# Kernel optimization log

Hardware: AMD Instinct MI355X
Metric: run time of the kernel (lower is better)

The kernel has to match this reference:

```python
import jax, jax.numpy as jnp
import numpy as np

EPS_COS = 1e-8   # nxn_cos_sim eps
SMOOTH = 1e-4    # DiceLoss smooth
EPS_DICE = 1e-7  # smp soft_dice_score clamp_min eps

BS, C, H, W = 8, 512, 128, 128
K = 512  # codebook / num classes


def setup_inputs() -> dict:
    key = jax.random.key(0)
    k1, k2, k3 = jax.random.split(key, 3)
    output = jax.random.normal(k1, (BS, C, H, W), dtype=jnp.float32)
    embeddings = jax.random.normal(k2, (K, C), dtype=jnp.float32)
    # ground-truth one-hot annotation (bs, K, h, w)
    gt_labels = jax.random.randint(k3, (BS, H, W), 0, K)
    ann_one_hot = jax.nn.one_hot(gt_labels, K, dtype=jnp.float32).transpose(0, 3, 1, 2)
    return {"output": output, "ann_one_hot": ann_one_hot, "embeddings": embeddings}


def reference(output, ann_one_hot, embeddings):
    bs, c, h, w = output.shape
    k = embeddings.shape[0]
    x = output.transpose(0, 2, 3, 1).reshape(-1, c)           # [N, C]
    # nxn cosine similarity [N, K]
    numerator = x @ embeddings.T
    a_l2 = jnp.sum(x * x, axis=1)                              # [N]
    b_l2 = jnp.sum(embeddings * embeddings, axis=1)            # [K]
    denominator = jnp.maximum(jnp.sqrt(a_l2[:, None] * b_l2[None, :]), EPS_COS)
    labels = jnp.argmax(numerator / denominator, axis=-1).reshape(bs, h, w)
    # ann_to_one_hot -> (bs, K, h, w)
    pred_one_hot = jax.nn.one_hot(labels, k, dtype=output.dtype).transpose(0, 3, 1, 2)
    # smp DiceLoss(mode='multilabel', smooth=1e-4, from_logits=False)
    yp = pred_one_hot.reshape(bs, k, -1)
    yt = ann_one_hot.reshape(bs, k, -1).astype(yp.dtype)
    dims = (0, 2)
    intersection = jnp.sum(yp * yt, axis=dims)                 # [K]
    cardinality = jnp.sum(yp + yt, axis=dims)                  # [K]
    score = (2.0 * intersection + SMOOTH) / jnp.maximum(cardinality + SMOOTH, EPS_DICE)
    loss = 1.0 - score
    present = (jnp.sum(yt, axis=dims) > 0).astype(loss.dtype)  # only classes present in GT
    return jnp.mean(loss * present)
```

## Files before the change

### kernel.cpp

```cpp
#include <hip/hip_runtime.h>
#include <hip/hip_bf16.h>

#define BSZ 8
#define CDIM 512
#define KDIM 512
#define HWSZ 16384
#define NPIX (BSZ*HWSZ)

using bf16x8 = __attribute__((ext_vector_type(8))) short;
using f32x4  = __attribute__((ext_vector_type(4))) float;
typedef unsigned long long u64;

__device__ __forceinline__ unsigned pack2bf16(float lo, float hi) {
  return (__builtin_bit_cast(unsigned, lo) >> 16) |
         (__builtin_bit_cast(unsigned, hi) & 0xFFFF0000u);
}

__device__ __forceinline__ void gload_lds16(const unsigned short* g, unsigned short* l) {
  __builtin_amdgcn_global_load_lds(
      (const __attribute__((address_space(1))) unsigned int*)g,
      (__attribute__((address_space(3))) unsigned int*)l, 16, 0, 0);
}

__global__ __launch_bounds__(64) void prep_emb_kernel(const float* __restrict__ E,
                                                      unsigned short* __restrict__ Eb,
                                                      unsigned short* __restrict__ EbT,
                                                      u64* __restrict__ keys,
                                                      float* __restrict__ counters,
                                                      int do_keys) {
  int k = blockIdx.x;
  int lane = threadIdx.x;
  if (do_keys) {
    u64* kp = keys + (size_t)k * 256;
    #pragma unroll
    for (int j = 0; j < 4; ++j) kp[lane + 64 * j] = 0ull;
  }
  if (k == 0) {
    uint4 z = {0u, 0u, 0u, 0u};
    #pragma unroll
    for (int j = 0; j < 6; ++j) ((uint4*)counters)[lane + 64 * j] = z;
  }
  const float4* row = (const float4*)(E + (size_t)k * CDIM);
  float4 v0 = row[lane * 2], v1 = row[lane * 2 + 1];
  float ss = v0.x*v0.x + v0.y*v0.y + v0.z*v0.z + v0.w*v0.w
           + v1.x*v1.x + v1.y*v1.y + v1.z*v1.z + v1.w*v1.w;
  #pragma unroll
  for (int d = 1; d < 64; d <<= 1) ss += __shfl_xor(ss, d, 64);
  float rinv = rsqrtf(fmaxf(ss, 1e-24f));
  float f[8] = {v0.x, v0.y, v0.z, v0.w, v1.x, v1.y, v1.z, v1.w};
  unsigned o[8];
  #pragma unroll
  for (int e = 0; e < 8; ++e) {
    float x = f[e] * rinv;
    unsigned u = __builtin_bit_cast(unsigned, x);
    o[e] = (u + 0x7FFFu + ((u >> 16) & 1u)) >> 16;
  }
  uint4 pack;
  pack.x = o[0] | (o[1] << 16);
  pack.y = o[2] | (o[3] << 16);
  pack.z = o[4] | (o[5] << 16);
  pack.w = o[6] | (o[7] << 16);
  ((uint4*)(Eb + (size_t)k * CDIM))[lane] = pack;
  int clsb = k >> 7, rowi = k & 127, cs = lane >> 2, q4 = lane & 3;
  *(uint4*)(EbT + (size_t)clsb * 65536 + cs * 4096 + rowi * 32 + q4 * 8) = pack;
}

__global__ __launch_bounds__(256) void gt_count_kernel(const float* __restrict__ ANN,
                                                       float* __restrict__ gt_count) {
  int slice = blockIdx.x;
  int k = slice & (KDIM - 1);
  const float4* p = (const float4*)(ANN + (size_t)slice * HWSZ);
  float s = 0.f;
  #pragma unroll
  for (int i = 0; i < 16; ++i) {
    float4 v = p[threadIdx.x + i * 256];
    s += v.x + v.y + v.z + v.w;
  }
  #pragma unroll
  for (int d = 1; d < 64; d <<= 1) s += __shfl_xor(s, d, 64);
  __shared__ float sw[4];
  if ((threadIdx.x & 63) == 0) sw[threadIdx.x >> 6] = s;
  __syncthreads();
  if (threadIdx.x == 0) {
    atomicAdd(&gt_count[k], sw[0] + sw[1] + sw[2] + sw[3]);
  }
}

__global__ __launch_bounds__(256) void transpose_v3_kernel(
    const float* __restrict__ X, unsigned short* __restrict__ XtT) {
  __shared__ unsigned int lds[16 * 1024];
  int t = threadIdx.x, w = t >> 6, l = t & 63;
  int bid = blockIdx.x;
  int pt = bid >> 4, ks = bid & 15;
  int px0 = pt << 10;
  int b = px0 >> 14, hw = px0 & (HWSZ - 1);
  const float* xb = X + ((size_t)b * CDIM + ks * 32 + 8 * w) * HWSZ + hw + 4 * l;

  float4 xv[8][4];
  #pragma unroll
  for (int r = 0; r < 8; ++r)
    #pragma unroll
    for (int s = 0; s < 4; ++s)
      xv[r][s] = *(const float4*)(xb + (size_t)r * HWSZ + s * 256);

  #pragma unroll
  for (int rp = 0; rp < 4; ++rp) {
    int cp = 4 * w + rp;
    int swz = (cp & 7) << 2;
    #pragma unroll
    for (int s = 0; s < 4; ++s) {
      unsigned pk[4];
      #pragma unroll
      for (int j = 0; j < 4; ++j)
        pk[j] = pack2bf16(((const float*)&xv[2 * rp][s])[j],
                          ((const float*)&xv[2 * rp + 1][s])[j]);
      *(uint4*)&lds[cp * 1024 + ((s * 256 + 4 * l) ^ swz)] = *(const uint4*)pk;
    }
  }
  __syncthreads();

  #pragma unroll
  for (int rr = 0; rr < 16; ++rr) {
    int ch = rr * 256 + t;
    int q4 = ch & 3, pxl = ch >> 2;
    unsigned o[4];
    #pragma unroll
    for (int j = 0; j < 4; ++j) {
      int cp = 4 * q4 + j;
      o[j] = lds[cp * 1024 + (pxl ^ ((cp & 7) << 2))];
    }
    int pxg = px0 + pxl;
    *(uint4*)(XtT + ((size_t)(pxg >> 7) * 16 + ks) * 4096 + (size_t)(pxg & 127) * 32 + q4 * 8)
        = *(const uint4*)o;
  }
}

__global__ __launch_bounds__(256, 4) void gemm_argmax_kernel(
    const unsigned short* __restrict__ XtT, const unsigned short* __restrict__ EbT,
    u64* __restrict__ keys) {
  __shared__ unsigned short As[2][128 * 32];
  __shared__ unsigned short Bs[2][128 * 32];
  int t = threadIdx.x;
  int lane = t & 63;
  int wv = t >> 6;
  int p15 = lane & 15, q = lane >> 4;
  int wr = wv >> 1, wc = wv & 1;
  int bid = (blockIdx.x & 7) * 512 + (blockIdx.x >> 3);
  int pxb  = bid >> 2;
  int clsb = bid & 3;
  int px0  = pxb * 128;
  int cls0 = clsb * 128;

  const unsigned short* Abase = XtT + (size_t)pxb * 65536;
  const unsigned short* Bbase = EbT + (size_t)clsb * 65536;
  int ubase = (t & ~63) * 8;
  #define STAGE(buf, i)                                                       \
    {                                                                         \
      _Pragma("unroll")                                                       \
      for (int j = 0; j < 2; ++j) {                                           \
        int ch = t + 256 * j;                                                 \
        gload_lds16(Abase + (size_t)(i) * 4096 + ch * 8, &As[buf][ubase + j * 2048]); \
        gload_lds16(Bbase + (size_t)(i) * 4096 + ch * 8, &Bs[buf][ubase + j * 2048]); \
      }                                                                       \
    }

  f32x4 acc[4][4];
  #pragma unroll
  for (int m = 0; m < 4; ++m)
    #pragma unroll
    for (int n = 0; n < 4; ++n)
      acc[m][n] = (f32x4){0.f, 0.f, 0.f, 0.f};

  STAGE(0, 0);
  for (int i = 0; i < 16; ++i) {
    int cur = i & 1;
    if (i < 15) STAGE(cur ^ 1, i + 1);
    __syncthreads();
    bf16x8 a[4], bfr[4];
    #pragma unroll
    for (int m = 0; m < 4; ++m)
      a[m] = *(bf16x8*)&As[cur][(wr * 64 + m * 16 + p15) * 32 + q * 8];
    #pragma unroll
    for (int n = 0; n < 4; ++n)
      bfr[n] = *(bf16x8*)&Bs[cur][(wc * 64 + n * 16 + p15) * 32 + q * 8];
    #pragma unroll
    for (int n = 0; n < 4; ++n)
      #pragma unroll
      for (int m = 0; m < 4; ++m)
        acc[m][n] = __builtin_amdgcn_mfma_f32_16x16x32_bf16(a[m], bfr[n], acc[m][n], 0, 0, 0);
    __syncthreads();
  }
  #undef STAGE

  #pragma unroll
  for (int m = 0; m < 4; ++m) {
    #pragma unroll
    for (int r = 0; r < 4; ++r) {
      float best = acc[m][0][r];
      int bn = 0;
      #pragma unroll
      for (int n = 1; n < 4; ++n) {
        float v = acc[m][n][r];
        if (v > best) { best = v; bn = n; }
      }
      int bk = cls0 + wc * 64 + bn * 16 + p15;
      #pragma unroll
      for (int d = 1; d < 16; d <<= 1) {
        float ov = __shfl_xor(best, d, 64);
        int   ok = __shfl_xor(bk, d, 64);
        if (ov > best || (ov == best && ok < bk)) { best = ov; bk = ok; }
      }
      if (p15 == 0) {
        int px = px0 + wr * 64 + m * 16 + q * 4 + r;
        unsigned u = __builtin_bit_cast(unsigned, best);
        unsigned ou = u ^ ((unsigned)((int)u >> 31) | 0x80000000u);
        u64 key = ((u64)ou << 32) | (unsigned)(511 - bk);
        atomicMax(&keys[px], key);
      }
    }
  }
}

__global__ __launch_bounds__(256) void count_kernel(
    const u64* __restrict__ keys, const float* __restrict__ ANN,
    int* __restrict__ pred_count, int* __restrict__ inter) {
  int px = blockIdx.x * 256 + threadIdx.x;
  u64 key = keys[px];
  int cls = 511 - (int)(unsigned)(key & 0xFFFFFFFFull);
  atomicAdd(&pred_count[cls], 1);
  int b = px >> 14, hw = px & (HWSZ - 1);
  float g = ANN[((size_t)b * KDIM + cls) * HWSZ + hw];
  if (g > 0.5f) atomicAdd(&inter[cls], 1);
}

__global__ __launch_bounds__(512) void final_kernel(
    const int* __restrict__ pred_count, const int* __restrict__ inter,
    const float* __restrict__ gt_count, float* __restrict__ out) {
  int k = threadIdx.x;
  float G = gt_count[k];
  float P = (float)pred_count[k];
  float I = (float)inter[k];
  float card  = P + G;
  float score = (2.f * I + 1e-4f) / fmaxf(card + 1e-4f, 1e-7f);
  float v = (G > 0.f) ? (1.f - score) : 0.f;
  #pragma unroll
  for (int d = 1; d < 64; d <<= 1) v += __shfl_xor(v, d, 64);
  __shared__ float sw[8];
  if ((k & 63) == 0) sw[k >> 6] = v;
  __syncthreads();
  if (k == 0) {
    float s = 0.f;
    #pragma unroll
    for (int i = 0; i < 8; ++i) s += sw[i];
    out[0] = s / (float)KDIM;
  }
}

__global__ __launch_bounds__(256, 1) void gemm_fb(
    const float* __restrict__ X, const float* __restrict__ ANN,
    const unsigned short* __restrict__ Eb,
    int* __restrict__ pred_count, int* __restrict__ inter) {
  int tid = threadIdx.x;
  int wv = tid >> 6;
  int lane = tid & 63;
  int p15 = lane & 15, q = lane >> 4;
  int pix0 = blockIdx.x * 64;
  int b = pix0 >> 14;
  int hw = pix0 & (HWSZ - 1);
  const float*          Xb = X  + (size_t)b * CDIM * HWSZ + hw + p15;
  const unsigned short* Ew = Eb + (size_t)(wv * 128) * CDIM;
  f32x4 acc[4][8];
  #pragma unroll
  for (int m = 0; m < 4; ++m)
    #pragma unroll
    for (int n = 0; n < 8; ++n)
      acc[m][n] = (f32x4){0.f, 0.f, 0.f, 0.f};
  for (int cs = 0; cs < 16; ++cs) {
    int c0 = cs * 32 + q * 8;
    bf16x8 a[4];
    #pragma unroll
    for (int m = 0; m < 4; ++m)
      #pragma unroll
      for (int e = 0; e < 8; ++e) {
        float x = Xb[(size_t)(c0 + e) * HWSZ + m * 16];
        a[m][e] = (short)(__builtin_bit_cast(unsigned, x) >> 16);
      }
    bf16x8 bfrag[8];
    #pragma unroll
    for (int n = 0; n < 8; ++n)
      bfrag[n] = *(const bf16x8*)(Ew + (size_t)(n * 16 + p15) * CDIM + cs * 32 + q * 8);
    #pragma unroll
    for (int n = 0; n < 8; ++n)
      #pragma unroll
      for (int m = 0; m < 4; ++m)
        acc[m][n] = __builtin_amdgcn_mfma_f32_16x16x32_bf16(a[m], bfrag[n], acc[m][n], 0, 0, 0);
  }
  __shared__ float s_v[4][64];
  __shared__ int   s_k[4][64];
  #pragma unroll
  for (int m = 0; m < 4; ++m)
    #pragma unroll
    for (int r = 0; r < 4; ++r) {
      float best = acc[m][0][r];
      int bn = 0;
      #pragma unroll
      for (int n = 1; n < 8; ++n) {
        float v = acc[m][n][r];
        if (v > best) { best = v; bn = n; }
      }
      int bk = wv * 128 + bn * 16 + p15;
      #pragma unroll
      for (int d = 1; d < 16; d <<= 1) {
        float ov = __shfl_xor(best, d, 64);
        int   ok = __shfl_xor(bk, d, 64);
        if (ov > best || (ov == best && ok < bk)) { best = ov; bk = ok; }
      }
      if (p15 == 0) {
        int p = m * 16 + q * 4 + r;
        s_v[wv][p] = best;
        s_k[wv][p] = bk;
      }
    }
  __syncthreads();
  if (tid < 64) {
    int p = tid;
    float best = s_v[0][p]; int bk = s_k[0][p];
    #pragma unroll
    for (int w = 1; w < 4; ++w) {
      float v = s_v[w][p]; int kk = s_k[w][p];
      if (v > best || (v == best && kk < bk)) { best = v; bk = kk; }
    }
    atomicAdd(&pred_count[bk], 1);
    float g = ANN[((size_t)b * KDIM + bk) * HWSZ + hw + p];
    if (g > 0.5f) atomicAdd(&inter[bk], 1);
  }
}

extern "C" void kernel_launch(void* const* d_in, const int* in_sizes, int n_in,
                              void* d_out, int out_size, void* d_ws, size_t ws_size,
                              hipStream_t stream) {
  const float* X   = (const float*)d_in[0];
  const float* ANN = (const float*)d_in[1];
  const float* E   = (const float*)d_in[2];

  char* base = (char*)d_ws;
  unsigned short* Eb  = (unsigned short*)base;
  unsigned short* EbT = (unsigned short*)(base + 524288);
  float* gt_count     = (float*)(base + 1048576);
  int*   pred_count   = (int*)  (base + 1048576 + 2048);
  int*   inter        = (int*)  (base + 1048576 + 4096);
  u64*   keys         = (u64*)  (base + 1048576 + 8192);
  unsigned short* XtT = (unsigned short*)(base + 4194304);

  size_t need = 4194304 + (size_t)NPIX * CDIM * 2;
  int big = (ws_size >= need) ? 1 : 0;

  prep_emb_kernel<<<KDIM, 64, 0, stream>>>(E, Eb, EbT, keys, gt_count, big);
  if (big) {
    gt_count_kernel<<<BSZ * KDIM, 256, 0, stream>>>(ANN, gt_count);
    transpose_v3_kernel<<<2048, 256, 0, stream>>>(X, XtT);
    gemm_argmax_kernel<<<4096, 256, 0, stream>>>(XtT, EbT, keys);
    count_kernel<<<NPIX / 256, 256, 0, stream>>>(keys, ANN, pred_count, inter);
  } else {
    gt_count_kernel<<<BSZ * KDIM, 256, 0, stream>>>(ANN, gt_count);
    gemm_fb<<<NPIX / 64, 256, 0, stream>>>(X, ANN, Eb, pred_count, inter);
  }
  final_kernel<<<1, 512, 0, stream>>>(pred_count, inter, gt_count, (float*)d_out);
}
```

Before: 286.6 us.

## Fuse GEMM-argmax, counting and GT-count into one kernel with full-K class tiles

```diff
diff --git a/kernel.cpp b/kernel.cpp
--- a/kernel.cpp
+++ b/kernel.cpp
@@ -25,16 +25,9 @@
 __global__ __launch_bounds__(64) void prep_emb_kernel(const float* __restrict__ E,
                                                       unsigned short* __restrict__ Eb,
                                                       unsigned short* __restrict__ EbT,
-                                                      u64* __restrict__ keys,
-                                                      float* __restrict__ counters,
-                                                      int do_keys) {
+                                                      float* __restrict__ counters) {
   int k = blockIdx.x;
   int lane = threadIdx.x;
-  if (do_keys) {
-    u64* kp = keys + (size_t)k * 256;
-    #pragma unroll
-    for (int j = 0; j < 4; ++j) kp[lane + 64 * j] = 0ull;
-  }
   if (k == 0) {
     uint4 z = {0u, 0u, 0u, 0u};
     #pragma unroll
@@ -61,8 +54,8 @@
   pack.z = o[4] | (o[5] << 16);
   pack.w = o[6] | (o[7] << 16);
   ((uint4*)(Eb + (size_t)k * CDIM))[lane] = pack;
-  int clsb = k >> 7, rowi = k & 127, cs = lane >> 2, q4 = lane & 3;
-  *(uint4*)(EbT + (size_t)clsb * 65536 + cs * 4096 + rowi * 32 + q4 * 8) = pack;
+  int ks = lane >> 2, q4 = lane & 3;
+  *(uint4*)(EbT + ((size_t)ks * 512 + k) * 32 + q4 * 8) = pack;
 }
 
 __global__ __launch_bounds__(256) void gt_count_kernel(const float* __restrict__ ANN,
@@ -81,9 +74,7 @@
   __shared__ float sw[4];
   if ((threadIdx.x & 63) == 0) sw[threadIdx.x >> 6] = s;
   __syncthreads();
-  if (threadIdx.x == 0) {
-    atomicAdd(&gt_count[k], sw[0] + sw[1] + sw[2] + sw[3]);
-  }
+  if (threadIdx.x == 0) atomicAdd(&gt_count[k], sw[0] + sw[1] + sw[2] + sw[3]);
 }
 
 __global__ __launch_bounds__(256) void transpose_v3_kernel(
@@ -130,38 +121,58 @@
       o[j] = lds[cp * 1024 + (pxl ^ ((cp & 7) << 2))];
     }
     int pxg = px0 + pxl;
-    *(uint4*)(XtT + ((size_t)(pxg >> 7) * 16 + ks) * 4096 + (size_t)(pxg & 127) * 32 + q4 * 8)
+    *(uint4*)(XtT + ((size_t)(pxg >> 6) * 16 + ks) * 2048 + (size_t)(pxg & 63) * 32 + q4 * 8)
         = *(const uint4*)o;
   }
 }
 
-__global__ __launch_bounds__(256, 4) void gemm_argmax_kernel(
+__global__ __launch_bounds__(512, 4) void mega_kernel(
     const unsigned short* __restrict__ XtT, const unsigned short* __restrict__ EbT,
-    u64* __restrict__ keys) {
-  __shared__ unsigned short As[2][128 * 32];
-  __shared__ unsigned short Bs[2][128 * 32];
+    const float* __restrict__ ANN, float* __restrict__ gt_count,
+    int* __restrict__ pred_count, int* __restrict__ inter) {
+  __shared__ unsigned short As[2][64 * 32];
+  __shared__ unsigned short Bs[2][512 * 32];
+  __shared__ float s_v[8][64];
+  __shared__ int   s_k[8][64];
+  __shared__ float sgt[8];
   int t = threadIdx.x;
-  int lane = t & 63;
-  int wv = t >> 6;
+  int bid = blockIdx.x;
+
+  if (bid & 1) {
+    int g = bid >> 1;
+    int which = t >> 8, tt = t & 255, w = t >> 6, lane = t & 63;
+    const float* Ap = ANN + (size_t)(2 * g + which) * HWSZ + tt * 4;
+    float s = 0.f;
+    #pragma unroll
+    for (int i = 0; i < 16; ++i) {
+      float4 v = *(const float4*)(Ap + (size_t)i * 1024);
+      s += (v.x + v.y) + (v.z + v.w);
+    }
+    #pragma unroll
+    for (int d = 1; d < 64; d <<= 1) s += __shfl_xor(s, d, 64);
+    if (lane == 0) sgt[w] = s;
+    __syncthreads();
+    if (t == 0)   atomicAdd(&gt_count[(2 * g)     & (KDIM - 1)], sgt[0] + sgt[1] + sgt[2] + sgt[3]);
+    if (t == 256) atomicAdd(&gt_count[(2 * g + 1) & (KDIM - 1)], sgt[4] + sgt[5] + sgt[6] + sgt[7]);
+    return;
+  }
+
+  int pxblk = bid >> 1;
+  int px0 = pxblk * 64;
+  int b = px0 >> 14, hw = px0 & (HWSZ - 1);
+  int lane = t & 63, wv = t >> 6;
   int p15 = lane & 15, q = lane >> 4;
-  int wr = wv >> 1, wc = wv & 1;
-  int bid = (blockIdx.x & 7) * 512 + (blockIdx.x >> 3);
-  int pxb  = bid >> 2;
-  int clsb = bid & 3;
-  int px0  = pxb * 128;
-  int cls0 = clsb * 128;
-
-  const unsigned short* Abase = XtT + (size_t)pxb * 65536;
-  const unsigned short* Bbase = EbT + (size_t)clsb * 65536;
-  int ubase = (t & ~63) * 8;
-  #define STAGE(buf, i)                                                       \
-    {                                                                         \
-      _Pragma("unroll")                                                       \
-      for (int j = 0; j < 2; ++j) {                                           \
-        int ch = t + 256 * j;                                                 \
-        gload_lds16(Abase + (size_t)(i) * 4096 + ch * 8, &As[buf][ubase + j * 2048]); \
-        gload_lds16(Bbase + (size_t)(i) * 4096 + ch * 8, &Bs[buf][ubase + j * 2048]); \
-      }                                                                       \
+
+  const unsigned short* Abase = XtT + (size_t)pxblk * 32768;
+  #define STAGE(buf, i)                                                               \
+    {                                                                                 \
+      _Pragma("unroll")                                                               \
+      for (int j = 0; j < 4; ++j)                                                     \
+        gload_lds16(EbT + (size_t)(i) * 16384 + ((size_t)t + 512 * j) * 8,            \
+                    &Bs[buf][(t & ~63) * 8 + j * 4096]);                              \
+      if (t < 256)                                                                    \
+        gload_lds16(Abase + (size_t)(i) * 2048 + (size_t)t * 8,                       \
+                    &As[buf][(t & ~63) * 8]);                                         \
     }
 
   f32x4 acc[4][4];
@@ -179,10 +190,10 @@
     bf16x8 a[4], bfr[4];
     #pragma unroll
     for (int m = 0; m < 4; ++m)
-      a[m] = *(bf16x8*)&As[cur][(wr * 64 + m * 16 + p15) * 32 + q * 8];
+      a[m] = *(bf16x8*)&As[cur][(m * 16 + p15) * 32 + q * 8];
     #pragma unroll
     for (int n = 0; n < 4; ++n)
-      bfr[n] = *(bf16x8*)&Bs[cur][(wc * 64 + n * 16 + p15) * 32 + q * 8];
+      bfr[n] = *(bf16x8*)&Bs[cur][(wv * 64 + n * 16 + p15) * 32 + q * 8];
     #pragma unroll
     for (int n = 0; n < 4; ++n)
       #pragma unroll
@@ -203,7 +214,7 @@
         float v = acc[m][n][r];
         if (v > best) { best = v; bn = n; }
       }
-      int bk = cls0 + wc * 64 + bn * 16 + p15;
+      int bk = wv * 64 + bn * 16 + p15;
       #pragma unroll
       for (int d = 1; d < 16; d <<= 1) {
         float ov = __shfl_xor(best, d, 64);
@@ -211,26 +222,25 @@
         if (ov > best || (ov == best && ok < bk)) { best = ov; bk = ok; }
       }
       if (p15 == 0) {
-        int px = px0 + wr * 64 + m * 16 + q * 4 + r;
-        unsigned u = __builtin_bit_cast(unsigned, best);
-        unsigned ou = u ^ ((unsigned)((int)u >> 31) | 0x80000000u);
-        u64 key = ((u64)ou << 32) | (unsigned)(511 - bk);
-        atomicMax(&keys[px], key);
-      }
-    }
-  }
-}
-
-__global__ __launch_bounds__(256) void count_kernel(
-    const u64* __restrict__ keys, const float* __restrict__ ANN,
-    int* __restrict__ pred_count, int* __restrict__ inter) {
-  int px = blockIdx.x * 256 + threadIdx.x;
-  u64 key = keys[px];
-  int cls = 511 - (int)(unsigned)(key & 0xFFFFFFFFull);
-  atomicAdd(&pred_count[cls], 1);
-  int b = px >> 14, hw = px & (HWSZ - 1);
-  float g = ANN[((size_t)b * KDIM + cls) * HWSZ + hw];
-  if (g > 0.5f) atomicAdd(&inter[cls], 1);
+        int p = m * 16 + q * 4 + r;
+        s_v[wv][p] = best;
+        s_k[wv][p] = bk;
+      }
+    }
+  }
+  __syncthreads();
+  if (t < 64) {
+    int p = t;
+    float best = s_v[0][p]; int bk = s_k[0][p];
+    #pragma unroll
+    for (int w = 1; w < 8; ++w) {
+      float v = s_v[w][p]; int kk = s_k[w][p];
+      if (v > best || (v == best && kk < bk)) { best = v; bk = kk; }
+    }
+    atomicAdd(&pred_count[bk], 1);
+    float g2 = ANN[((size_t)b * KDIM + bk) * HWSZ + hw + p];
+    if (g2 > 0.5f) atomicAdd(&inter[bk], 1);
+  }
 }
 
 __global__ __launch_bounds__(512) void final_kernel(
@@ -349,18 +359,15 @@
   float* gt_count     = (float*)(base + 1048576);
   int*   pred_count   = (int*)  (base + 1048576 + 2048);
   int*   inter        = (int*)  (base + 1048576 + 4096);
-  u64*   keys         = (u64*)  (base + 1048576 + 8192);
   unsigned short* XtT = (unsigned short*)(base + 4194304);
 
   size_t need = 4194304 + (size_t)NPIX * CDIM * 2;
   int big = (ws_size >= need) ? 1 : 0;
 
-  prep_emb_kernel<<<KDIM, 64, 0, stream>>>(E, Eb, EbT, keys, gt_count, big);
+  prep_emb_kernel<<<KDIM, 64, 0, stream>>>(E, Eb, EbT, gt_count);
   if (big) {
-    gt_count_kernel<<<BSZ * KDIM, 256, 0, stream>>>(ANN, gt_count);
     transpose_v3_kernel<<<2048, 256, 0, stream>>>(X, XtT);
-    gemm_argmax_kernel<<<4096, 256, 0, stream>>>(XtT, EbT, keys);
-    count_kernel<<<NPIX / 256, 256, 0, stream>>>(keys, ANN, pred_count, inter);
+    mega_kernel<<<4096, 512, 0, stream>>>(XtT, EbT, ANN, gt_count, pred_count, inter);
   } else {
     gt_count_kernel<<<BSZ * KDIM, 256, 0, stream>>>(ANN, gt_count);
     gemm_fb<<<NPIX / 64, 256, 0, stream>>>(X, ANN, Eb, pred_count, inter);
```

Result: slower. 324.8 us (+13.3%).
